# Optimization experiments

Measured on AMD Instinct MI355X. Metric: run time of the kernel, lower is better.

Reference implementation:

```python
import jax, jax.numpy as jnp
import numpy as np

WS = 7        # window size
SHIFT = 3     # shift size (ws // 2)
NH = 8        # num heads
EPS = 1e-5


def _ln(x, g, b):
    m = x.mean(-1, keepdims=True)
    v = ((x - m) ** 2).mean(-1, keepdims=True)
    return (x - m) / jnp.sqrt(v + EPS) * g + b


def setup_inputs() -> dict:
    key = jax.random.key(0)
    B, Hh, Ww, C = 8, 112, 112, 256
    N = Hh * Ww
    hidden = 4 * C
    ks = jax.random.split(key, 12)
    x = jax.random.normal(ks[0], (B, N, C), jnp.float32)

    # --- standard Swin shifted-window additive attention mask ---
    img_mask = np.zeros((Hh, Ww), np.float32)
    cnt = 0
    for hs in (slice(0, -WS), slice(-WS, -SHIFT), slice(-SHIFT, None)):
        for wsl in (slice(0, -WS), slice(-WS, -SHIFT), slice(-SHIFT, None)):
            img_mask[hs, wsl] = cnt
            cnt += 1
    mw = img_mask.reshape(Hh // WS, WS, Ww // WS, WS).transpose(0, 2, 1, 3).reshape(-1, WS * WS)
    am = mw[:, None, :] - mw[:, :, None]
    mask_matrix = jnp.asarray(np.where(am != 0, -100.0, 0.0).astype(np.float32))  # (nW, 49, 49)

    s = 0.02
    return dict(
        x=x,
        mask_matrix=mask_matrix,
        norm1_g=jnp.ones((C,), jnp.float32),
        norm1_b=jnp.zeros((C,), jnp.float32),
        qkv_w=jax.random.normal(ks[1], (C, 3 * C), jnp.float32) * s,
        qkv_b=jnp.zeros((3 * C,), jnp.float32),
        proj_w=jax.random.normal(ks[2], (C, C), jnp.float32) * s,
        proj_b=jnp.zeros((C,), jnp.float32),
        norm2_g=jnp.ones((C,), jnp.float32),
        norm2_b=jnp.zeros((C,), jnp.float32),
        fc1_w=jax.random.normal(ks[3], (C, hidden), jnp.float32) * s,
        fc1_b=jnp.zeros((hidden,), jnp.float32),
        fc2_w=jax.random.normal(ks[4], (hidden, C), jnp.float32) * s,
        fc2_b=jnp.zeros((C,), jnp.float32),
        H=112,
        W=112,
    )


def reference(x, mask_matrix, norm1_g, norm1_b, qkv_w, qkv_b, proj_w, proj_b,
              norm2_g, norm2_b, fc1_w, fc1_b, fc2_w, fc2_b, H, W):
    B, N, C = x.shape
    hd = C // NH
    scale = hd ** (-0.5)
    wsws = WS * WS

    # --- SwinLocallyGroupedAttn on norm1(x) ---
    xa = _ln(x, norm1_g, norm1_b).reshape(B, H, W, C)
    pad_r = (WS - W % WS) % WS
    pad_b = (WS - H % WS) % WS
    if pad_r > 0 or pad_b > 0:
        xa = jnp.pad(xa, ((0, 0), (0, pad_b), (0, pad_r), (0, 0)))
    Hp, Wp = H + pad_b, W + pad_r
    xa = jnp.roll(xa, shift=(-SHIFT, -SHIFT), axis=(1, 2))
    h_, w_ = Hp // WS, Wp // WS
    nW = h_ * w_
    # window partition: (B*nW, ws*ws, C)
    xw = xa.reshape(B, h_, WS, w_, WS, C).transpose(0, 1, 3, 2, 4, 5).reshape(B * nW, wsws, C)
    qkv = (xw @ qkv_w + qkv_b).reshape(B * nW, wsws, 3, NH, hd).transpose(2, 0, 3, 1, 4)
    q, k, v = qkv[0], qkv[1], qkv[2]          # (B*nW, NH, wsws, hd)
    attn = jnp.einsum('wnqd,wnkd->wnqk', q, k) * scale
    attn = attn.reshape(B, nW, NH, wsws, wsws) + mask_matrix[None, :, None]
    attn = jax.nn.softmax(attn, axis=-1).reshape(B * nW, NH, wsws, wsws)
    out = jnp.einsum('wnqk,wnkd->wnqd', attn, v).transpose(0, 2, 1, 3).reshape(B * nW, wsws, C)
    out = out @ proj_w + proj_b
    # window reverse + un-shift + crop
    out = out.reshape(B, h_, w_, WS, WS, C).transpose(0, 1, 3, 2, 4, 5).reshape(B, Hp, Wp, C)
    out = jnp.roll(out, shift=(SHIFT, SHIFT), axis=(1, 2))
    out = out[:, :H, :W, :].reshape(B, N, C)
    x = x + out

    # --- MLP branch ---
    h = _ln(x, norm2_g, norm2_b)
    h = jax.nn.gelu(h @ fc1_w + fc1_b, approximate=False)
    x = x + (h @ fc2_w + fc2_b)
    return x
```

## Files before the change

kernel.cpp:

```cpp
#include <hip/hip_runtime.h>
#include <hip/hip_bf16.h>
#include <cstdint>

#define WS_    7
#define SHIFT_ 3
#define NH_    8
#define HD_    32
#define C_     256
#define H_     112
#define W_     112
#define B_     8
#define WSQ    49
#define ROWS   100352
#define HIDDEN 1024

typedef __attribute__((ext_vector_type(8))) short short8;
typedef __attribute__((ext_vector_type(4))) float f32x4;

__device__ inline ushort f2bf(float f){
  uint32_t u = __float_as_uint(f);
  u += 0x7fffu + ((u >> 16) & 1u);
  return (ushort)(u >> 16);
}
__device__ inline float bf2f(ushort s){ return __uint_as_float(((uint32_t)s) << 16); }

__device__ inline int row2tok(int r){
  int w  = r / WSQ, p = r - w * WSQ;
  int b  = w >> 8, wi = w & 255;
  int wh = wi >> 4, ww = wi & 15;
  int i  = p / WS_, j = p - i * WS_;
  int h  = wh * WS_ + i + SHIFT_; if (h >= H_) h -= H_;
  int wc = ww * WS_ + j + SHIFT_; if (wc >= W_) wc -= W_;
  return b * (H_ * W_) + h * W_ + wc;
}

__global__ void transpose_cast(const float* __restrict__ in, ushort* __restrict__ out,
                               int K, int N){
  int idx = blockIdx.x * 256 + threadIdx.x;
  if (idx >= K * N) return;
  int k = idx / N, n = idx - k * N;
  out[(size_t)n * K + k] = f2bf(in[idx]);
}

template<bool GATHER>
__global__ __launch_bounds__(256) void ln_kernel(const float* __restrict__ x,
    const float* __restrict__ g, const float* __restrict__ b, ushort* __restrict__ out)
{
  int wave = threadIdx.x >> 6, lane = threadIdx.x & 63;
  int r = blockIdx.x * 4 + wave;
  int t = GATHER ? row2tok(r) : r;
  const float4 v = *(const float4*)(x + (size_t)t * C_ + lane * 4);
  float s  = v.x + v.y + v.z + v.w;
  float s2 = v.x * v.x + v.y * v.y + v.z * v.z + v.w * v.w;
  #pragma unroll
  for (int m = 32; m; m >>= 1){ s += __shfl_xor(s, m); s2 += __shfl_xor(s2, m); }
  float mean = s * (1.f / C_);
  float inv  = rsqrtf(fmaxf(s2 * (1.f / C_) - mean * mean, 0.f) + 1e-5f);
  int c0 = lane * 4;
  ushort4 o;
  o.x = f2bf((v.x - mean) * inv * g[c0 + 0] + b[c0 + 0]);
  o.y = f2bf((v.y - mean) * inv * g[c0 + 1] + b[c0 + 1]);
  o.z = f2bf((v.z - mean) * inv * g[c0 + 2] + b[c0 + 2]);
  o.w = f2bf((v.w - mean) * inv * g[c0 + 3] + b[c0 + 3]);
  *(ushort4*)(out + (size_t)r * C_ + c0) = o;
}

__device__ inline void gll16(const void* g, void* l){
  __builtin_amdgcn_global_load_lds(
      (__attribute__((address_space(1))) void*)g,
      (__attribute__((address_space(3))) void*)l, 16, 0, 0);
}

template<int EPI>
__global__ __launch_bounds__(256, 2) void gemm128(
    const ushort* __restrict__ A,
    const ushort* __restrict__ Bt,
    const float*  __restrict__ bias,
    void*         __restrict__ Cout,
    const float*  __restrict__ resid,
    int M, int N, int K)
{
  __shared__ __align__(16) ushort lA[128 * 32];
  __shared__ __align__(16) ushort lB[128 * 32];
  const int tid  = threadIdx.x;
  const int m0   = blockIdx.x * 128, n0 = blockIdx.y * 128;
  const int wave = tid >> 6, lane = tid & 63;
  const int wr   = wave >> 1, wc = wave & 1;
  const int la   = lane & 15, lg = lane >> 4;

  f32x4 acc[4][4] = {};

  const int r0 = tid >> 2, kp = (tid & 3) * 8;
  const ushort* pA0 = A  + (size_t)(m0 + r0)      * K + kp;
  const ushort* pA1 = A  + (size_t)(m0 + r0 + 64) * K + kp;
  const ushort* pB0 = Bt + (size_t)(n0 + r0)      * K + kp;
  const ushort* pB1 = Bt + (size_t)(n0 + r0 + 64) * K + kp;
  ushort* lA0 = lA + tid * 8;  ushort* lA1 = lA + (tid + 256) * 8;
  ushort* lB0 = lB + tid * 8;  ushort* lB1 = lB + (tid + 256) * 8;

  for (int k0 = 0; k0 < K; k0 += 32){
    gll16(pA0 + k0, lA0);
    gll16(pA1 + k0, lA1);
    gll16(pB0 + k0, lB0);
    gll16(pB1 + k0, lB1);
    __syncthreads();
    short8 af[4], bfr[4];
    #pragma unroll
    for (int i = 0; i < 4; i++) af[i]  = *(const short8*)&lA[(wr * 64 + i * 16 + la) * 32 + lg * 8];
    #pragma unroll
    for (int j = 0; j < 4; j++) bfr[j] = *(const short8*)&lB[(wc * 64 + j * 16 + la) * 32 + lg * 8];
    #pragma unroll
    for (int i = 0; i < 4; i++)
      #pragma unroll
      for (int j = 0; j < 4; j++)
        acc[i][j] = __builtin_amdgcn_mfma_f32_16x16x32_bf16(af[i], bfr[j], acc[i][j], 0, 0, 0);
    __syncthreads();
  }

  #pragma unroll
  for (int i = 0; i < 4; i++){
    #pragma unroll
    for (int j = 0; j < 4; j++){
      int col = n0 + wc * 64 + j * 16 + la;
      float bs = bias[col];
      #pragma unroll
      for (int q = 0; q < 4; q++){
        int row = m0 + wr * 64 + i * 16 + lg * 4 + q;
        float v = acc[i][j][q] + bs;
        if (EPI == 0){
          ((ushort*)Cout)[(size_t)row * N + col] = f2bf(v);
        } else if (EPI == 1){
          int t = row2tok(row);
          size_t o = (size_t)t * C_ + col;
          ((float*)Cout)[o] = resid[o] + v;
        } else if (EPI == 2){
          float gx = 0.5f * v * (1.f + erff(v * 0.70710678118f));
          ((ushort*)Cout)[(size_t)row * N + col] = f2bf(gx);
        } else {
          size_t o = (size_t)row * C_ + col;
          ((float*)Cout)[o] = resid[o] + v;
        }
      }
    }
  }
}

__global__ __launch_bounds__(256, 2) void attn_kernel(const ushort* __restrict__ qkv,
    const float* __restrict__ mask, ushort* __restrict__ out)
{
  __shared__ __align__(16) ushort P [4][64 * 72];
  __shared__ __align__(16) ushort VT[4][32 * 72];
  const int wave = threadIdx.x >> 6, lane = threadIdx.x & 63;
  const int gid  = blockIdx.x * 4 + wave;
  const int w    = gid >> 3, head = gid & 7;
  const int la   = lane & 15, lg = lane >> 4;
  const ushort* qb = qkv + (size_t)w * WSQ * 768 + head * HD_;
  const short8 z8 = {0,0,0,0,0,0,0,0};

  {
    ushort4 z4 = {0,0,0,0};
    for (int idx = lane; idx < (32 * 72) / 4; idx += 64) ((ushort4*)VT[wave])[idx] = z4;
    for (int idx = lane; idx < WSQ * 4; idx += 64){
      int row = idx >> 2, db = idx & 3;
      short8 vv = *(const short8*)&qb[(size_t)row * 768 + 512 + db * 8];
      #pragma unroll
      for (int e = 0; e < 8; e++) VT[wave][(db * 8 + e) * 72 + row] = ((ushort*)&vv)[e];
    }
  }

  short8 qf[4], kf[4];
  #pragma unroll
  for (int i = 0; i < 4; i++){
    int m = i * 16 + la;
    qf[i] = (m < WSQ) ? *(const short8*)&qb[(size_t)m * 768 +       lg * 8] : z8;
    kf[i] = (m < WSQ) ? *(const short8*)&qb[(size_t)m * 768 + 256 + lg * 8] : z8;
  }

  f32x4 s[4][4] = {};
  #pragma unroll
  for (int i = 0; i < 4; i++)
    #pragma unroll
    for (int j = 0; j < 4; j++)
      s[i][j] = __builtin_amdgcn_mfma_f32_16x16x32_bf16(qf[i], kf[j], s[i][j], 0, 0, 0);

  const float* mrow = mask + (size_t)(w & 255) * WSQ * WSQ;
  const float scale = 0.17677669529663687f;
  float rinv[4][4];
  #pragma unroll
  for (int i = 0; i < 4; i++){
    #pragma unroll
    for (int q = 0; q < 4; q++){
      int m = i * 16 + lg * 4 + q;
      float pv[4]; float mx = -1e30f;
      #pragma unroll
      for (int j = 0; j < 4; j++){
        int n = j * 16 + la;
        float val = (m < WSQ && n < WSQ) ? s[i][j][q] * scale + mrow[m * WSQ + n] : -1e30f;
        pv[j] = val; mx = fmaxf(mx, val);
      }
      #pragma unroll
      for (int msk = 1; msk < 16; msk <<= 1) mx = fmaxf(mx, __shfl_xor(mx, msk));
      float sum = 0.f;
      #pragma unroll
      for (int j = 0; j < 4; j++){ float e = __expf(pv[j] - mx); pv[j] = e; sum += e; }
      #pragma unroll
      for (int msk = 1; msk < 16; msk <<= 1) sum += __shfl_xor(sum, msk);
      rinv[i][q] = 1.f / sum;
      #pragma unroll
      for (int j = 0; j < 4; j++) P[wave][m * 72 + j * 16 + la] = f2bf(pv[j]);
    }
  }

  f32x4 o[4][2] = {};
  #pragma unroll
  for (int kk = 0; kk < 2; kk++){
    short8 pf[4], vf[2];
    #pragma unroll
    for (int i = 0; i < 4; i++)  pf[i]  = *(const short8*)&P [wave][(i  * 16 + la) * 72 + kk * 32 + lg * 8];
    #pragma unroll
    for (int jn = 0; jn < 2; jn++) vf[jn] = *(const short8*)&VT[wave][(jn * 16 + la) * 72 + kk * 32 + lg * 8];
    #pragma unroll
    for (int i = 0; i < 4; i++)
      #pragma unroll
      for (int jn = 0; jn < 2; jn++)
        o[i][jn] = __builtin_amdgcn_mfma_f32_16x16x32_bf16(pf[i], vf[jn], o[i][jn], 0, 0, 0);
  }

  ushort* ob = out + (size_t)w * WSQ * C_ + head * HD_;
  #pragma unroll
  for (int i = 0; i < 4; i++)
    #pragma unroll
    for (int jn = 0; jn < 2; jn++)
      #pragma unroll
      for (int q = 0; q < 4; q++){
        int m = i * 16 + lg * 4 + q;
        if (m < WSQ) ob[(size_t)m * C_ + jn * 16 + la] = f2bf(o[i][jn][q] * rinv[i][q]);
      }
}

extern "C" void kernel_launch(void* const* d_in, const int* in_sizes, int n_in,
                              void* d_out, int out_size, void* d_ws, size_t ws_size,
                              hipStream_t stream)
{
  const float* x      = (const float*)d_in[0];
  const float* mask   = (const float*)d_in[1];
  const float* n1g    = (const float*)d_in[2];
  const float* n1b    = (const float*)d_in[3];
  const float* qkv_w  = (const float*)d_in[4];
  const float* qkv_b  = (const float*)d_in[5];
  const float* proj_w = (const float*)d_in[6];
  const float* proj_b = (const float*)d_in[7];
  const float* n2g    = (const float*)d_in[8];
  const float* n2b    = (const float*)d_in[9];
  const float* fc1_w  = (const float*)d_in[10];
  const float* fc1_b  = (const float*)d_in[11];
  const float* fc2_w  = (const float*)d_in[12];
  const float* fc2_b  = (const float*)d_in[13];

  char* ws = (char*)d_ws;
  ushort* R1 = (ushort*)ws;
  ushort* R2 = (ushort*)(ws + 51380224);
  float*  x2 = (float*) (ws + 51380224 + 205520896);
  ushort* wqT = (ushort*)(ws + 51380224 + 205520896 + 102760448);
  ushort* wpT = wqT + 768 * 256;
  ushort* w1T = wpT + 256 * 256;
  ushort* w2T = w1T + 1024 * 256;

  transpose_cast<<<(256 * 768  + 255) / 256, 256, 0, stream>>>(qkv_w,  wqT, 256, 768);
  transpose_cast<<<(256 * 256  + 255) / 256, 256, 0, stream>>>(proj_w, wpT, 256, 256);
  transpose_cast<<<(256 * 1024 + 255) / 256, 256, 0, stream>>>(fc1_w,  w1T, 256, 1024);
  transpose_cast<<<(1024 * 256 + 255) / 256, 256, 0, stream>>>(fc2_w,  w2T, 1024, 256);

  ln_kernel<true><<<ROWS / 4, 256, 0, stream>>>(x, n1g, n1b, R1);
  gemm128<0><<<dim3(ROWS / 128, 6), 256, 0, stream>>>(R1, wqT, qkv_b, R2, nullptr, ROWS, 768, 256);
  attn_kernel<<<(2048 * 8) / 4, 256, 0, stream>>>(R2, mask, R1);
  gemm128<1><<<dim3(ROWS / 128, 2), 256, 0, stream>>>(R1, wpT, proj_b, x2, x, ROWS, 256, 256);
  ln_kernel<false><<<ROWS / 4, 256, 0, stream>>>(x2, n2g, n2b, R1);
  gemm128<2><<<dim3(ROWS / 128, 8), 256, 0, stream>>>(R1, w1T, fc1_b, R2, nullptr, ROWS, 1024, 256);
  gemm128<3><<<dim3(ROWS / 128, 2), 256, 0, stream>>>(R2, w2T, fc2_b, d_out, x2, ROWS, 256, 1024);
}
```

Before: 716.7 us.

## Widen GEMM tiles to 128x256 with double-buffered LDS and XCD-aware block remap

Replaces the 128x128 GEMM with a 512-thread 128x256 tile kernel that double-buffers the A/B LDS tiles, issuing the next K-slice's global-to-LDS loads before computing the current one and dropping one barrier per iteration. Block IDs are remapped so consecutive logical tiles land on the same XCD (blockIdx mod 8), which should improve L2 reuse of A rows across column tiles. The wider tile halves A re-reads. In exchange, LDS use doubles and the occupancy hint rises to 4 blocks of 512 threads, which may not be reachable and could add register pressure.

```diff
diff --git a/kernel.cpp b/kernel.cpp
--- a/kernel.cpp
+++ b/kernel.cpp
@@ -22,7 +22,6 @@
   u += 0x7fffu + ((u >> 16) & 1u);
   return (ushort)(u >> 16);
 }
-__device__ inline float bf2f(ushort s){ return __uint_as_float(((uint32_t)s) << 16); }
 
 __device__ inline int row2tok(int r){
   int w  = r / WSQ, p = r - w * WSQ;
@@ -72,49 +71,61 @@
 }
 
 template<int EPI>
-__global__ __launch_bounds__(256, 2) void gemm128(
+__global__ __launch_bounds__(512, 4) void gemmW(
     const ushort* __restrict__ A,
     const ushort* __restrict__ Bt,
     const float*  __restrict__ bias,
     void*         __restrict__ Cout,
     const float*  __restrict__ resid,
-    int M, int N, int K)
-{
-  __shared__ __align__(16) ushort lA[128 * 32];
-  __shared__ __align__(16) ushort lB[128 * 32];
+    int M, int N, int K, int nN)
+{
+  __shared__ __align__(16) ushort lA[2][128 * 32];
+  __shared__ __align__(16) ushort lB[2][256 * 32];
   const int tid  = threadIdx.x;
-  const int m0   = blockIdx.x * 128, n0 = blockIdx.y * 128;
+
+  const int cpx  = gridDim.x >> 3;
+  const int lid  = (blockIdx.x & 7) * cpx + (blockIdx.x >> 3);
+  const int rowb = lid / nN, colb = lid - rowb * nN;
+  const int m0   = rowb * 128, n0 = colb * 256;
+
   const int wave = tid >> 6, lane = tid & 63;
-  const int wr   = wave >> 1, wc = wave & 1;
+  const int wr   = wave >> 2, wc = wave & 3;
   const int la   = lane & 15, lg = lane >> 4;
 
   f32x4 acc[4][4] = {};
 
   const int r0 = tid >> 2, kp = (tid & 3) * 8;
-  const ushort* pA0 = A  + (size_t)(m0 + r0)      * K + kp;
-  const ushort* pA1 = A  + (size_t)(m0 + r0 + 64) * K + kp;
-  const ushort* pB0 = Bt + (size_t)(n0 + r0)      * K + kp;
-  const ushort* pB1 = Bt + (size_t)(n0 + r0 + 64) * K + kp;
-  ushort* lA0 = lA + tid * 8;  ushort* lA1 = lA + (tid + 256) * 8;
-  ushort* lB0 = lB + tid * 8;  ushort* lB1 = lB + (tid + 256) * 8;
-
-  for (int k0 = 0; k0 < K; k0 += 32){
-    gll16(pA0 + k0, lA0);
-    gll16(pA1 + k0, lA1);
-    gll16(pB0 + k0, lB0);
-    gll16(pB1 + k0, lB1);
-    __syncthreads();
+  const ushort* gA  = A  + (size_t)(m0 + r0)       * K + kp;
+  const ushort* gB0 = Bt + (size_t)(n0 + r0)       * K + kp;
+  const ushort* gB1 = Bt + (size_t)(n0 + r0 + 128) * K + kp;
+
+  const int nt = K >> 5;
+  int buf = 0;
+
+  gll16(gA,  &lA[0][tid * 8]);
+  gll16(gB0, &lB[0][tid * 8]);
+  gll16(gB1, &lB[0][(tid + 512) * 8]);
+  __syncthreads();
+
+  for (int t = 0; t < nt; ++t){
+    if (t + 1 < nt){
+      const int k0 = (t + 1) * 32;
+      gll16(gA  + k0, &lA[buf ^ 1][tid * 8]);
+      gll16(gB0 + k0, &lB[buf ^ 1][tid * 8]);
+      gll16(gB1 + k0, &lB[buf ^ 1][(tid + 512) * 8]);
+    }
     short8 af[4], bfr[4];
     #pragma unroll
-    for (int i = 0; i < 4; i++) af[i]  = *(const short8*)&lA[(wr * 64 + i * 16 + la) * 32 + lg * 8];
-    #pragma unroll
-    for (int j = 0; j < 4; j++) bfr[j] = *(const short8*)&lB[(wc * 64 + j * 16 + la) * 32 + lg * 8];
+    for (int i = 0; i < 4; i++) af[i]  = *(const short8*)&lA[buf][(wr * 64 + i * 16 + la) * 32 + lg * 8];
+    #pragma unroll
+    for (int j = 0; j < 4; j++) bfr[j] = *(const short8*)&lB[buf][(wc * 64 + j * 16 + la) * 32 + lg * 8];
     #pragma unroll
     for (int i = 0; i < 4; i++)
       #pragma unroll
       for (int j = 0; j < 4; j++)
         acc[i][j] = __builtin_amdgcn_mfma_f32_16x16x32_bf16(af[i], bfr[j], acc[i][j], 0, 0, 0);
     __syncthreads();
+    buf ^= 1;
   }
 
   #pragma unroll
@@ -272,10 +283,10 @@
   transpose_cast<<<(1024 * 256 + 255) / 256, 256, 0, stream>>>(fc2_w,  w2T, 1024, 256);
 
   ln_kernel<true><<<ROWS / 4, 256, 0, stream>>>(x, n1g, n1b, R1);
-  gemm128<0><<<dim3(ROWS / 128, 6), 256, 0, stream>>>(R1, wqT, qkv_b, R2, nullptr, ROWS, 768, 256);
+  gemmW<0><<<784 * 3, 512, 0, stream>>>(R1, wqT, qkv_b, R2, nullptr, ROWS, 768, 256, 3);
   attn_kernel<<<(2048 * 8) / 4, 256, 0, stream>>>(R2, mask, R1);
-  gemm128<1><<<dim3(ROWS / 128, 2), 256, 0, stream>>>(R1, wpT, proj_b, x2, x, ROWS, 256, 256);
+  gemmW<1><<<784 * 1, 512, 0, stream>>>(R1, wpT, proj_b, x2, x, ROWS, 256, 256, 1);
   ln_kernel<false><<<ROWS / 4, 256, 0, stream>>>(x2, n2g, n2b, R1);
-  gemm128<2><<<dim3(ROWS / 128, 8), 256, 0, stream>>>(R1, w1T, fc1_b, R2, nullptr, ROWS, 1024, 256);
-  gemm128<3><<<dim3(ROWS / 128, 2), 256, 0, stream>>>(R2, w2T, fc2_b, d_out, x2, ROWS, 256, 1024);
-}
+  gemmW<2><<<784 * 4, 512, 0, stream>>>(R1, w1T, fc1_b, R2, nullptr, ROWS, 1024, 256, 4);
+  gemmW<3><<<784 * 1, 512, 0, stream>>>(R2, w2T, fc2_b, d_out, x2, ROWS, 256, 1024, 1);
+}
```

Result: faster. 674.4 us (-5.9%).
